# Kernel tuning notes

Measured on AMD Instinct MI355X. Metric: run time of the kernel, lower is better.

The kernel has to match this reference:

```python
import jax, jax.numpy as jnp
import numpy as np

N_NODES = 50000
N_EDGES = 800000
D_IN = 256
D_OUT = 128


def setup_inputs() -> dict:
    key = jax.random.key(0)
    k1, k2, k3, k4, k5, k6 = jax.random.split(key, 6)
    std = 1.0 / np.sqrt(D_OUT)
    return {
        "feat": jax.random.normal(k1, (N_NODES, D_IN), dtype=jnp.float32),
        "adj_row": jax.random.randint(k2, (N_EDGES,), 0, N_NODES, dtype=jnp.int32),
        "adj_col": jax.random.randint(k3, (N_EDGES,), 0, N_NODES, dtype=jnp.int32),
        "adj_vals": jax.random.uniform(k4, (N_EDGES,), dtype=jnp.float32),
        "weight": jax.random.uniform(k5, (D_IN, D_OUT), minval=-std, maxval=std, dtype=jnp.float32),
        "bias": jax.random.uniform(k6, (D_OUT,), minval=-std, maxval=std, dtype=jnp.float32),
    }


def reference(feat, adj_row, adj_col, adj_vals, weight, bias):
    # support = feat @ W            [N, D_out]
    support = jnp.matmul(feat, weight)
    # output = spmm(adj, support): out[r] += vals[e] * support[c] for edge e=(r,c)
    messages = adj_vals[:, None] * support[adj_col]  # [E, D_out]
    output = jax.ops.segment_sum(messages, adj_row, num_segments=N_NODES)
    return output + bias
```

## Files before the change

### kernel.cpp

```cpp
#include <hip/hip_runtime.h>

#define N_NODES 50000
#define N_EDGES 800000
#define D_IN 256
#define D_OUT 128
#define ROWS_PER_GRP 6250

typedef __attribute__((ext_vector_type(8))) short bf16x8;
typedef __attribute__((ext_vector_type(4))) float f32x4;

__device__ inline unsigned short f32_to_bf16_rne(float x) {
    unsigned u = __float_as_uint(x);
    unsigned r = (u + 0x7FFFu + ((u >> 16) & 1u)) >> 16;
    return (unsigned short)r;
}
__device__ inline float bf16_to_f32(unsigned short h) {
    return __uint_as_float(((unsigned)h) << 16);
}

__global__ __launch_bounds__(256)
void pack_b_kernel(const float* __restrict__ W, short* __restrict__ Bhi,
                   short* __restrict__ Blo) {
    const int gid = blockIdx.x * 256 + threadIdx.x;
    if (gid >= 8 * 8 * 64) return;
    const int lane = gid & 63;
    const int slot = gid >> 6;
    const int ct = slot & 7, ks = slot >> 3;
    const int krow = ks * 32 + (lane >> 4) * 8;
    const int col  = ct * 16 + (lane & 15);
    bf16x8 hi, lo;
    #pragma unroll
    for (int j = 0; j < 8; ++j) {
        float v = W[(size_t)(krow + j) * D_OUT + col];
        unsigned short h = f32_to_bf16_rne(v);
        float rem = v - bf16_to_f32(h);
        hi[j] = (short)h;
        lo[j] = (short)f32_to_bf16_rne(rem);
    }
    *reinterpret_cast<bf16x8*>(Bhi + (size_t)gid * 8) = hi;
    *reinterpret_cast<bf16x8*>(Blo + (size_t)gid * 8) = lo;
}

__global__ __launch_bounds__(256)
void gemm_mfma_kernel(const float* __restrict__ A, const short* __restrict__ Bhi,
                      const short* __restrict__ Blo, float* __restrict__ C, int M) {
    const int tid  = threadIdx.x;
    const int w    = tid >> 6;
    const int lane = tid & 63;
    const int m0   = blockIdx.x * 64 + w * 16;
    const int r    = m0 + (lane & 15);
    const int kgrp = lane >> 4;

    f32x4 acc[8];
    #pragma unroll
    for (int ct = 0; ct < 8; ++ct) acc[ct] = (f32x4){0.f, 0.f, 0.f, 0.f};

    const bool valid = (r < M);
    const float* arow = A + (size_t)r * D_IN + kgrp * 8;
    const bf16x8* bh8 = reinterpret_cast<const bf16x8*>(Bhi);
    const bf16x8* bl8 = reinterpret_cast<const bf16x8*>(Blo);

    #pragma unroll
    for (int ks = 0; ks < 8; ++ks) {
        float av[8];
        if (valid) {
            *reinterpret_cast<float4*>(av)     = *reinterpret_cast<const float4*>(arow + ks * 32);
            *reinterpret_cast<float4*>(av + 4) = *reinterpret_cast<const float4*>(arow + ks * 32 + 4);
        } else {
            #pragma unroll
            for (int j = 0; j < 8; ++j) av[j] = 0.f;
        }
        bf16x8 ahi, alo;
        #pragma unroll
        for (int j = 0; j < 8; ++j) {
            unsigned short h = f32_to_bf16_rne(av[j]);
            ahi[j] = (short)h;
            alo[j] = (short)f32_to_bf16_rne(av[j] - bf16_to_f32(h));
        }
        #pragma unroll
        for (int ct = 0; ct < 8; ++ct) {
            bf16x8 bhi = bh8[(ks * 8 + ct) * 64 + lane];
            bf16x8 blo = bl8[(ks * 8 + ct) * 64 + lane];
            acc[ct] = __builtin_amdgcn_mfma_f32_16x16x32_bf16(ahi, bhi, acc[ct], 0, 0, 0);
            acc[ct] = __builtin_amdgcn_mfma_f32_16x16x32_bf16(alo, bhi, acc[ct], 0, 0, 0);
            acc[ct] = __builtin_amdgcn_mfma_f32_16x16x32_bf16(ahi, blo, acc[ct], 0, 0, 0);
        }
    }

    #pragma unroll
    for (int reg = 0; reg < 4; ++reg) {
        const int g = m0 + kgrp * 4 + reg;
        if (g < M) {
            #pragma unroll
            for (int ct = 0; ct < 8; ++ct)
                C[(size_t)g * D_OUT + ct * 16 + (lane & 15)] = acc[ct][reg];
        }
    }
}

__global__ __launch_bounds__(256)
void scatter_bins_kernel(const int* __restrict__ row, const int* __restrict__ col,
                         const float* __restrict__ vals, int* __restrict__ cnt,
                         int2* __restrict__ bins, int stride, int cap) {
    const int g  = blockIdx.x & 7;
    const int nb = gridDim.x >> 3;
    const int bg = blockIdx.x >> 3;
    for (int e = bg * 256 + threadIdx.x; e < N_EDGES; e += nb * 256) {
        int r = row[e];
        if (r / ROWS_PER_GRP == g) {
            int p = atomicAdd(&cnt[r * stride], 1);
            if (p < cap)
                bins[(size_t)r * cap + p] = make_int2(col[e], __float_as_int(vals[e]));
        }
    }
}

__global__ __launch_bounds__(256)
void gather_bins_kernel(const int* __restrict__ cnt, const int2* __restrict__ bins,
                        const float* __restrict__ sup, const float* __restrict__ bias,
                        float* __restrict__ out, int stride, int cap) {
    const int wid  = (blockIdx.x * 256 + threadIdx.x) >> 6;
    const int lane = threadIdx.x & 63;
    if (wid >= N_NODES) return;

    int n = cnt[wid * stride];
    if (n > cap) n = cap;
    const int2* eb = bins + (size_t)wid * cap;
    const float2* sup2 = reinterpret_cast<const float2*>(sup);

    float2 a0 = make_float2(0.f, 0.f), a1 = a0, a2 = a0, a3 = a0;
    int j = 0;
    for (; j + 3 < n; j += 4) {
        int2 e0 = eb[j],     e1 = eb[j + 1];
        int2 e2 = eb[j + 2], e3 = eb[j + 3];
        float v0 = __int_as_float(e0.y), v1 = __int_as_float(e1.y);
        float v2 = __int_as_float(e2.y), v3 = __int_as_float(e3.y);
        float2 s0 = sup2[(size_t)e0.x * 64 + lane];
        float2 s1 = sup2[(size_t)e1.x * 64 + lane];
        float2 s2 = sup2[(size_t)e2.x * 64 + lane];
        float2 s3 = sup2[(size_t)e3.x * 64 + lane];
        a0.x = fmaf(v0, s0.x, a0.x);  a0.y = fmaf(v0, s0.y, a0.y);
        a1.x = fmaf(v1, s1.x, a1.x);  a1.y = fmaf(v1, s1.y, a1.y);
        a2.x = fmaf(v2, s2.x, a2.x);  a2.y = fmaf(v2, s2.y, a2.y);
        a3.x = fmaf(v3, s3.x, a3.x);  a3.y = fmaf(v3, s3.y, a3.y);
    }
    for (; j < n; ++j) {
        int2 e0 = eb[j];
        float v = __int_as_float(e0.y);
        float2 s = sup2[(size_t)e0.x * 64 + lane];
        a0.x = fmaf(v, s.x, a0.x);  a0.y = fmaf(v, s.y, a0.y);
    }

    float2 b = reinterpret_cast<const float2*>(bias)[lane];
    float2 rr = make_float2(a0.x + a1.x + a2.x + a3.x + b.x,
                            a0.y + a1.y + a2.y + a3.y + b.y);
    reinterpret_cast<float2*>(out)[(size_t)wid * 64 + lane] = rr;
}

__global__ __launch_bounds__(256)
void hist_kernel(const int* __restrict__ row, int* __restrict__ cnt, int stride) {
    for (int e = blockIdx.x * blockDim.x + threadIdx.x; e < N_EDGES;
         e += gridDim.x * blockDim.x)
        atomicAdd(&cnt[row[e] * stride], 1);
}

#define SCAN_BLOCKS 200

__global__ __launch_bounds__(256)
void scan_partial(const int* __restrict__ cnt, int* __restrict__ partials, int stride) {
    __shared__ int sdata[256];
    const int t = threadIdx.x;
    const int i = blockIdx.x * 256 + t;
    sdata[t] = (i < N_NODES) ? cnt[i * stride] : 0;
    __syncthreads();
    #pragma unroll
    for (int off = 128; off > 0; off >>= 1) {
        if (t < off) sdata[t] += sdata[t + off];
        __syncthreads();
    }
    if (t == 0) partials[blockIdx.x] = sdata[0];
}

__global__ __launch_bounds__(256)
void scan_base(const int* __restrict__ partials, int* __restrict__ base) {
    __shared__ int buf[256];
    const int t = threadIdx.x;
    int v = (t < SCAN_BLOCKS) ? partials[t] : 0;
    buf[t] = v;
    __syncthreads();
    #pragma unroll
    for (int off = 1; off < 256; off <<= 1) {
        int u = (t >= off) ? buf[t - off] : 0;
        __syncthreads();
        buf[t] += u;
        __syncthreads();
    }
    if (t < SCAN_BLOCKS) base[t] = buf[t] - v;
}

__global__ __launch_bounds__(256)
void scan_final(int* __restrict__ cnt, const int* __restrict__ base,
                int* __restrict__ row_ptr, int stride) {
    __shared__ int buf[256];
    const int t = threadIdx.x;
    const int i = blockIdx.x * 256 + t;
    int v = (i < N_NODES) ? cnt[i * stride] : 0;
    buf[t] = v;
    __syncthreads();
    #pragma unroll
    for (int off = 1; off < 256; off <<= 1) {
        int u = (t >= off) ? buf[t - off] : 0;
        __syncthreads();
        buf[t] += u;
        __syncthreads();
    }
    int excl = buf[t] - v + base[blockIdx.x];
    if (i < N_NODES) {
        row_ptr[i] = excl;
        cnt[i * stride] = excl;
    }
    if (i == N_NODES) row_ptr[N_NODES] = N_EDGES;
}

__global__ __launch_bounds__(256)
void scatter_kernel(const int* __restrict__ row, const int* __restrict__ col,
                    const float* __restrict__ vals, int* __restrict__ cursor,
                    int2* __restrict__ edge_s, int stride) {
    for (int e = blockIdx.x * blockDim.x + threadIdx.x; e < N_EDGES;
         e += gridDim.x * blockDim.x) {
        int p = atomicAdd(&cursor[row[e] * stride], 1);
        edge_s[p] = make_int2(col[e], __float_as_int(vals[e]));
    }
}

__global__ __launch_bounds__(256)
void gather_kernel(const int* __restrict__ row_ptr, const int2* __restrict__ edge_s,
                   const float* __restrict__ sup, const float* __restrict__ bias,
                   float* __restrict__ out) {
    const int wid  = (blockIdx.x * 256 + threadIdx.x) >> 6;
    const int lane = threadIdx.x & 63;
    if (wid >= N_NODES) return;

    const float2* sup2 = reinterpret_cast<const float2*>(sup);
    const int start = row_ptr[wid];
    const int end   = row_ptr[wid + 1];

    float2 a0 = make_float2(0.f, 0.f), a1 = a0, a2 = a0, a3 = a0;
    int j = start;
    for (; j + 3 < end; j += 4) {
        int2 e0 = edge_s[j],     e1 = edge_s[j + 1];
        int2 e2 = edge_s[j + 2], e3 = edge_s[j + 3];
        float v0 = __int_as_float(e0.y), v1 = __int_as_float(e1.y);
        float v2 = __int_as_float(e2.y), v3 = __int_as_float(e3.y);
        float2 s0 = sup2[(size_t)e0.x * 64 + lane];
        float2 s1 = sup2[(size_t)e1.x * 64 + lane];
        float2 s2 = sup2[(size_t)e2.x * 64 + lane];
        float2 s3 = sup2[(size_t)e3.x * 64 + lane];
        a0.x = fmaf(v0, s0.x, a0.x);  a0.y = fmaf(v0, s0.y, a0.y);
        a1.x = fmaf(v1, s1.x, a1.x);  a1.y = fmaf(v1, s1.y, a1.y);
        a2.x = fmaf(v2, s2.x, a2.x);  a2.y = fmaf(v2, s2.y, a2.y);
        a3.x = fmaf(v3, s3.x, a3.x);  a3.y = fmaf(v3, s3.y, a3.y);
    }
    for (; j < end; ++j) {
        int2 e0 = edge_s[j];
        float v = __int_as_float(e0.y);
        float2 s = sup2[(size_t)e0.x * 64 + lane];
        a0.x = fmaf(v, s.x, a0.x);  a0.y = fmaf(v, s.y, a0.y);
    }

    float2 b = reinterpret_cast<const float2*>(bias)[lane];
    float2 rr = make_float2(a0.x + a1.x + a2.x + a3.x + b.x,
                            a0.y + a1.y + a2.y + a3.y + b.y);
    reinterpret_cast<float2*>(out)[(size_t)wid * 64 + lane] = rr;
}

extern "C" void kernel_launch(void* const* d_in, const int* in_sizes, int n_in,
                              void* d_out, int out_size, void* d_ws, size_t ws_size,
                              hipStream_t stream) {
    const float* feat     = (const float*)d_in[0];
    const int*   adj_row  = (const int*)d_in[1];
    const int*   adj_col  = (const int*)d_in[2];
    const float* adj_vals = (const float*)d_in[3];
    const float* weight   = (const float*)d_in[4];
    const float* bias     = (const float*)d_in[5];
    float* out = (float*)d_out;

    char* bb = (char*)d_ws;
    float* support = (float*)bb;
    short* Bhi     = (short*)(bb + 25600000);
    short* Blo     = (short*)(bb + 25665536);
    const size_t common_end = 25731072;

    const int STRIDE = 16;
    int* cnt   = (int*)(bb + common_end);
    int2* bins = (int2*)(bb + common_end + 3200000);
    const size_t need_cap64 = common_end + 3200000 + (size_t)N_NODES * 64 * 8;
    const size_t need_cap48 = common_end + 3200000 + (size_t)N_NODES * 48 * 8;

    pack_b_kernel<<<16, 256, 0, stream>>>(weight, Bhi, Blo);
    gemm_mfma_kernel<<<(N_NODES + 63) / 64, 256, 0, stream>>>(feat, Bhi, Blo,
                                                              support, N_NODES);

    int cap = 0;
    if (ws_size >= need_cap64) cap = 64;
    else if (ws_size >= need_cap48) cap = 48;

    if (cap > 0) {
        hipMemsetAsync(cnt, 0, (size_t)N_NODES * STRIDE * sizeof(int), stream);
        scatter_bins_kernel<<<3128, 256, 0, stream>>>(adj_row, adj_col, adj_vals,
                                                      cnt, bins, STRIDE, cap);
        const int blocks = (N_NODES * 64 + 255) / 256;
        gather_bins_kernel<<<blocks, 256, 0, stream>>>(cnt, bins, support, bias,
                                                       out, STRIDE, cap);
    } else {
        int2* edge_s   = (int2*)(bb + common_end);
        int*  row_ptr  = (int*)(bb + common_end + 6400000);
        int*  partials = (int*)(bb + common_end + 6600004);
        int*  base     = partials + 256;
        const size_t fixed_end = common_end + 6600004 + 2048;
        int*  cursor   = (int*)(bb + fixed_end);

        int stride = 0;
        if      (ws_size >= fixed_end + (size_t)N_NODES * 16 * 4) stride = 16;
        else if (ws_size >= fixed_end + (size_t)N_NODES * 8 * 4)  stride = 8;
        else if (ws_size >= fixed_end + (size_t)N_NODES * 4 * 4)  stride = 4;
        else if (ws_size >= fixed_end + (size_t)N_NODES * 2 * 4)  stride = 2;
        else                                                       stride = 1;

        hipMemsetAsync(cursor, 0, (size_t)N_NODES * stride * sizeof(int), stream);
        hist_kernel<<<3125, 256, 0, stream>>>(adj_row, cursor, stride);
        scan_partial<<<SCAN_BLOCKS, 256, 0, stream>>>(cursor, partials, stride);
        scan_base<<<1, 256, 0, stream>>>(partials, base);
        scan_final<<<SCAN_BLOCKS, 256, 0, stream>>>(cursor, base, row_ptr, stride);
        scatter_kernel<<<3125, 256, 0, stream>>>(adj_row, adj_col, adj_vals,
                                                 cursor, edge_s, stride);
        const int blocks = (N_NODES * 64 + 255) / 256;
        gather_kernel<<<blocks, 256, 0, stream>>>(row_ptr, edge_s,
                                                  support, bias, out);
    }
}
```

Before: 232.4 us.

## Slice gather by column groups and pack edge counters densely

The gather kernel now splits each output row across 8 blocks by 16-column slices. Each wave handles one row, and its 4 sub-groups of 16 lanes walk alternate edges, with the partial sums combined by shuffles. The per-row counters drop the 16-int padding stride and are packed densely, which shrinks the memset and the counter footprint. The aim is more parallelism and a spread of scattered support reads across blocks. The cost is 8x more reads of the bin entries, scalar 64-byte segment loads instead of float2 rows, and denser atomic contention on the counters.

```diff
diff --git a/kernel.cpp b/kernel.cpp
--- a/kernel.cpp
+++ b/kernel.cpp
@@ -101,14 +101,14 @@
 __global__ __launch_bounds__(256)
 void scatter_bins_kernel(const int* __restrict__ row, const int* __restrict__ col,
                          const float* __restrict__ vals, int* __restrict__ cnt,
-                         int2* __restrict__ bins, int stride, int cap) {
+                         int2* __restrict__ bins, int cap) {
     const int g  = blockIdx.x & 7;
     const int nb = gridDim.x >> 3;
     const int bg = blockIdx.x >> 3;
     for (int e = bg * 256 + threadIdx.x; e < N_EDGES; e += nb * 256) {
         int r = row[e];
         if (r / ROWS_PER_GRP == g) {
-            int p = atomicAdd(&cnt[r * stride], 1);
+            int p = atomicAdd(&cnt[r], 1);
             if (p < cap)
                 bins[(size_t)r * cap + p] = make_int2(col[e], __float_as_int(vals[e]));
         }
@@ -116,45 +116,35 @@
 }
 
 __global__ __launch_bounds__(256)
-void gather_bins_kernel(const int* __restrict__ cnt, const int2* __restrict__ bins,
-                        const float* __restrict__ sup, const float* __restrict__ bias,
-                        float* __restrict__ out, int stride, int cap) {
-    const int wid  = (blockIdx.x * 256 + threadIdx.x) >> 6;
-    const int lane = threadIdx.x & 63;
-    if (wid >= N_NODES) return;
-
-    int n = cnt[wid * stride];
+void gather_sliced_kernel(const int* __restrict__ cnt, const int2* __restrict__ bins,
+                          const float* __restrict__ sup, const float* __restrict__ bias,
+                          float* __restrict__ out, int cap) {
+    const int tid  = threadIdx.x;
+    const int wave = tid >> 6;
+    const int lane = tid & 63;
+    const int g    = blockIdx.x & 7;
+    const int row  = (blockIdx.x >> 3) * 4 + wave;
+    if (row >= N_NODES) return;
+    const int d0 = g * 16;
+    const int c  = lane & 15;
+    const int s  = lane >> 4;
+
+    int n = cnt[row];
     if (n > cap) n = cap;
-    const int2* eb = bins + (size_t)wid * cap;
-    const float2* sup2 = reinterpret_cast<const float2*>(sup);
-
-    float2 a0 = make_float2(0.f, 0.f), a1 = a0, a2 = a0, a3 = a0;
-    int j = 0;
-    for (; j + 3 < n; j += 4) {
-        int2 e0 = eb[j],     e1 = eb[j + 1];
-        int2 e2 = eb[j + 2], e3 = eb[j + 3];
-        float v0 = __int_as_float(e0.y), v1 = __int_as_float(e1.y);
-        float v2 = __int_as_float(e2.y), v3 = __int_as_float(e3.y);
-        float2 s0 = sup2[(size_t)e0.x * 64 + lane];
-        float2 s1 = sup2[(size_t)e1.x * 64 + lane];
-        float2 s2 = sup2[(size_t)e2.x * 64 + lane];
-        float2 s3 = sup2[(size_t)e3.x * 64 + lane];
-        a0.x = fmaf(v0, s0.x, a0.x);  a0.y = fmaf(v0, s0.y, a0.y);
-        a1.x = fmaf(v1, s1.x, a1.x);  a1.y = fmaf(v1, s1.y, a1.y);
-        a2.x = fmaf(v2, s2.x, a2.x);  a2.y = fmaf(v2, s2.y, a2.y);
-        a3.x = fmaf(v3, s3.x, a3.x);  a3.y = fmaf(v3, s3.y, a3.y);
-    }
-    for (; j < n; ++j) {
-        int2 e0 = eb[j];
-        float v = __int_as_float(e0.y);
-        float2 s = sup2[(size_t)e0.x * 64 + lane];
-        a0.x = fmaf(v, s.x, a0.x);  a0.y = fmaf(v, s.y, a0.y);
-    }
-
-    float2 b = reinterpret_cast<const float2*>(bias)[lane];
-    float2 rr = make_float2(a0.x + a1.x + a2.x + a3.x + b.x,
-                            a0.y + a1.y + a2.y + a3.y + b.y);
-    reinterpret_cast<float2*>(out)[(size_t)wid * 64 + lane] = rr;
+    const int2* eb = bins + (size_t)row * cap;
+
+    float acc = 0.f;
+    for (int j = 0; j < n; j += 4) {
+        const int jj = j + s;
+        const bool ok = (jj < n);
+        int2 e = ok ? eb[jj] : make_int2(0, 0);
+        float v = ok ? __int_as_float(e.y) : 0.f;
+        acc = fmaf(v, sup[(size_t)e.x * D_OUT + d0 + c], acc);
+    }
+    acc += __shfl_xor(acc, 16);
+    acc += __shfl_xor(acc, 32);
+    if (s == 0)
+        out[(size_t)row * D_OUT + d0 + c] = acc + bias[d0 + c];
 }
 
 __global__ __launch_bounds__(256)
@@ -291,11 +281,10 @@
     short* Blo     = (short*)(bb + 25665536);
     const size_t common_end = 25731072;
 
-    const int STRIDE = 16;
-    int* cnt   = (int*)(bb + common_end);
-    int2* bins = (int2*)(bb + common_end + 3200000);
-    const size_t need_cap64 = common_end + 3200000 + (size_t)N_NODES * 64 * 8;
-    const size_t need_cap48 = common_end + 3200000 + (size_t)N_NODES * 48 * 8;
+    int*  cnt  = (int*)(bb + common_end);
+    int2* bins = (int2*)(bb + common_end + 200000);
+    const size_t need_cap64 = common_end + 200000 + (size_t)N_NODES * 64 * 8;
+    const size_t need_cap48 = common_end + 200000 + (size_t)N_NODES * 48 * 8;
 
     pack_b_kernel<<<16, 256, 0, stream>>>(weight, Bhi, Blo);
     gemm_mfma_kernel<<<(N_NODES + 63) / 64, 256, 0, stream>>>(feat, Bhi, Blo,
@@ -306,12 +295,11 @@
     else if (ws_size >= need_cap48) cap = 48;
 
     if (cap > 0) {
-        hipMemsetAsync(cnt, 0, (size_t)N_NODES * STRIDE * sizeof(int), stream);
+        hipMemsetAsync(cnt, 0, (size_t)N_NODES * sizeof(int), stream);
         scatter_bins_kernel<<<3128, 256, 0, stream>>>(adj_row, adj_col, adj_vals,
-                                                      cnt, bins, STRIDE, cap);
-        const int blocks = (N_NODES * 64 + 255) / 256;
-        gather_bins_kernel<<<blocks, 256, 0, stream>>>(cnt, bins, support, bias,
-                                                       out, STRIDE, cap);
+                                                      cnt, bins, cap);
+        gather_sliced_kernel<<<100000, 256, 0, stream>>>(cnt, bins, support, bias,
+                                                         out, cap);
     } else {
         int2* edge_s   = (int2*)(bb + common_end);
         int*  row_ptr  = (int*)(bb + common_end + 6400000);
```

New measurement: 374.0 us. +60.9%, slower.
